# Kernel optimization log

Hardware: AMD Instinct MI355X
Metric: run time of the kernel (lower is better)

Reference implementation:

```python
import jax, jax.numpy as jnp
import numpy as np

NUM_ANCHORS = 3
NUM_CLASSES = 3
NUM_BB_ATTR = 9  # x, y, z, h, w, l, im, re, conf
EXP_CLAMP = 1000.0

_ANCHORS = np.array([[11.4, 8.6, 38.7, 0.0, 1.0],
                     [25.4, 11.2, 52.0, 0.0, 1.0],
                     [41.9, 16.2, 75.2, 0.0, 1.0]], dtype=np.float32)


def setup_inputs() -> dict:
    key = jax.random.key(0)
    B, G = 32, 152
    C = NUM_ANCHORS * (NUM_BB_ATTR + NUM_CLASSES)  # 36
    x = jax.random.normal(key, (B, C, G, G), dtype=jnp.float32)
    anchors = jnp.asarray(_ANCHORS)
    return {"x": x, "anchors": anchors, "img_size": 608}


def reference(x, anchors, img_size):
    B, _, G, _ = x.shape
    nA, nC, nbb = NUM_ANCHORS, NUM_CLASSES, NUM_BB_ATTR
    stride = jnp.asarray(img_size, x.dtype) / G

    # [B, nA, 9+nC, G, G] -> [B, nA, G, G, 9+nC]
    pred = x.reshape(B, nA, nbb + nC, G, G).transpose(0, 1, 3, 4, 2)

    pred_x = jax.nn.sigmoid(pred[..., 0])
    pred_y = jax.nn.sigmoid(pred[..., 1])
    pred_z = jax.nn.sigmoid(pred[..., 2])
    pred_h = pred[..., 3]
    pred_w = pred[..., 4]
    pred_l = pred[..., 5]
    pred_im = pred[..., 6]
    pred_re = pred[..., 7]
    pred_conf = jax.nn.sigmoid(pred[..., 8])
    pred_cls = jax.nn.sigmoid(pred[..., 9:])

    # grid offsets: grid_x varies along last (x) axis, grid_y along row axis
    g = jnp.arange(G, dtype=x.dtype)
    grid_x = g[None, None, None, :]   # [1,1,1,G] broadcasts over rows
    grid_y = g[None, None, :, None]   # [1,1,G,1] broadcasts over cols

    scaled = jnp.concatenate([anchors[:, :3] / stride, anchors[:, 3:]], axis=1)
    anchor_h = scaled[:, 0].reshape(1, nA, 1, 1)
    anchor_w = scaled[:, 1].reshape(1, nA, 1, 1)
    anchor_l = scaled[:, 2].reshape(1, nA, 1, 1)

    bx = pred_x + grid_x
    by = pred_y + grid_y
    bz = pred_z
    bh = jnp.minimum(jnp.exp(pred_h), EXP_CLAMP) * anchor_h
    bw = jnp.minimum(jnp.exp(pred_w), EXP_CLAMP) * anchor_w
    bl = jnp.minimum(jnp.exp(pred_l), EXP_CLAMP) * anchor_l

    N = nA * G * G
    flat = lambda t: t.reshape(B, N, 1)
    output = jnp.concatenate([
        flat(bx) * stride, flat(by) * stride,   # xy in image units
        flat(bz),
        flat(bh) * stride, flat(bw) * stride, flat(bl) * stride,
        flat(pred_im), flat(pred_re),
        flat(pred_conf),
        pred_cls.reshape(B, N, nC),
    ], axis=-1)  # [B, nA*G*G, 9+nC]
    return output
```

## Files before the change

### kernel.cpp

```cpp
#include <hip/hip_runtime.h>
#include <math.h>

#define GDIM 152
#define NA 3
#define GG (GDIM * GDIM)
#define EXP_CLAMP 1000.0f

__device__ __forceinline__ float sigmoidf(float v) {
    return 1.0f / (1.0f + __expf(-v));
}

__global__ __launch_bounds__(256) void yolo_decode_v4s(
    const float* __restrict__ x,
    const float* __restrict__ anchors,
    const int* __restrict__ img_size_p,
    float* __restrict__ out,
    int total4)
{
    int tid = blockIdx.x * blockDim.x + threadIdx.x;
    if (tid >= total4) return;
    int base = tid * 4;

    float stride = (float)(*img_size_p) / (float)GDIM;
    float inv_s = 1.0f / stride;

    int gx0 = base % GDIM;
    int t1  = base / GDIM;
    int gy  = t1 % GDIM;
    int t2  = t1 / GDIM;
    int a   = t2 % NA;
    float gyf = (float)gy;

    const float4* ip = (const float4*)(x + (size_t)t2 * 12 * GG + (size_t)gy * GDIM + gx0);
    const int PS = GG / 4;

    float4 r0  = ip[0 * PS];
    float4 r1  = ip[1 * PS];
    float4 r2  = ip[2 * PS];
    float4 r3  = ip[3 * PS];
    float4 r4  = ip[4 * PS];
    float4 r5  = ip[5 * PS];
    float4 r6  = ip[6 * PS];
    float4 r7  = ip[7 * PS];
    float4 r8  = ip[8 * PS];
    float4 r9  = ip[9 * PS];
    float4 r10 = ip[10 * PS];
    float4 r11 = ip[11 * PS];

    float ah4 = anchors[a * 5 + 0] * inv_s * stride;
    float aw4 = anchors[a * 5 + 1] * inv_s * stride;
    float al4 = anchors[a * 5 + 2] * inv_s * stride;

    float4* op = (float4*)(out + (size_t)base * 12);

#define PROC(J, C)                                                        \
    do {                                                                  \
        float4 o0, o1, o2;                                                \
        o0.x = (sigmoidf(r0.C) + (float)(gx0 + J)) * stride;              \
        o0.y = (sigmoidf(r1.C) + gyf) * stride;                           \
        o0.z = sigmoidf(r2.C);                                            \
        o0.w = fminf(__expf(r3.C), EXP_CLAMP) * ah4;                      \
        o1.x = fminf(__expf(r4.C), EXP_CLAMP) * aw4;                      \
        o1.y = fminf(__expf(r5.C), EXP_CLAMP) * al4;                      \
        o1.z = r6.C;                                                      \
        o1.w = r7.C;                                                      \
        o2.x = sigmoidf(r8.C);                                            \
        o2.y = sigmoidf(r9.C);                                            \
        o2.z = sigmoidf(r10.C);                                           \
        o2.w = sigmoidf(r11.C);                                           \
        op[(J) * 3 + 0] = o0;                                             \
        op[(J) * 3 + 1] = o1;                                             \
        op[(J) * 3 + 2] = o2;                                             \
    } while (0)

    PROC(0, x);
    PROC(1, y);
    PROC(2, z);
    PROC(3, w);
#undef PROC
}

extern "C" void kernel_launch(void* const* d_in, const int* in_sizes, int n_in,
                              void* d_out, int out_size, void* d_ws, size_t ws_size,
                              hipStream_t stream) {
    const float* x        = (const float*)d_in[0];
    const float* anchors  = (const float*)d_in[1];
    const int*   img_size = (const int*)d_in[2];
    float*       out      = (float*)d_out;

    const int B = 32;
    const int total4 = (B * NA * GG) / 4;
    const int block = 256;
    const int grid = (total4 + block - 1) / block;

    yolo_decode_v4s<<<grid, block, 0, stream>>>(x, anchors, img_size, out, total4);
}
```

Baseline: 225.5 us.

## Stage outputs through swizzled LDS for fully coalesced global stores

Each block now handles a 1024-cell tile. Threads write their computed 12-float records into XOR-swizzled shared memory, then after a barrier the block writes the tile out as contiguous float4 stores. This replaces per-thread strided 192-byte writes with coalesced ones. In exchange it uses 48 KB of LDS per block, which limits occupancy, and adds a barrier plus LDS traffic.

```diff
diff --git a/kernel.cpp b/kernel.cpp
--- a/kernel.cpp
+++ b/kernel.cpp
@@ -5,33 +5,38 @@
 #define NA 3
 #define GG (GDIM * GDIM)
 #define EXP_CLAMP 1000.0f
+#define TILE 1024
+#define NTHREADS 256
 
 __device__ __forceinline__ float sigmoidf(float v) {
     return 1.0f / (1.0f + __expf(-v));
 }
 
-__global__ __launch_bounds__(256) void yolo_decode_v4s(
+__device__ __forceinline__ int swz(int e) { return e ^ ((e >> 3) & 7); }
+
+__global__ __launch_bounds__(NTHREADS) void yolo_decode_lds(
     const float* __restrict__ x,
     const float* __restrict__ anchors,
     const int* __restrict__ img_size_p,
-    float* __restrict__ out,
-    int total4)
+    float* __restrict__ out)
 {
-    int tid = blockIdx.x * blockDim.x + threadIdx.x;
-    if (tid >= total4) return;
-    int base = tid * 4;
+    __shared__ float4 sh[3][TILE];
 
-    float stride = (float)(*img_size_p) / (float)GDIM;
-    float inv_s = 1.0f / stride;
+    const int t = threadIdx.x;
+    const int tilebase = blockIdx.x * TILE;
 
-    int gx0 = base % GDIM;
-    int t1  = base / GDIM;
-    int gy  = t1 % GDIM;
-    int t2  = t1 / GDIM;
-    int a   = t2 % NA;
-    float gyf = (float)gy;
+    const float stride = (float)(*img_size_p) / (float)GDIM;
+    const float inv_s = 1.0f / stride;
 
-    const float4* ip = (const float4*)(x + (size_t)t2 * 12 * GG + (size_t)gy * GDIM + gx0);
+    const int cbase = tilebase + 4 * t;
+    const unsigned t2 = (unsigned)cbase / (unsigned)GG;
+    const int pos = cbase - (int)t2 * GG;
+    const int gy  = pos / GDIM;
+    const int gx0 = pos - gy * GDIM;
+    const int a   = (int)(t2 % 3u);
+    const float gyf = (float)gy;
+
+    const float4* ip = (const float4*)x + (size_t)(t2 * 12u) * (GG / 4) + (pos >> 2);
     const int PS = GG / 4;
 
     float4 r0  = ip[0 * PS];
@@ -47,30 +52,29 @@
     float4 r10 = ip[10 * PS];
     float4 r11 = ip[11 * PS];
 
-    float ah4 = anchors[a * 5 + 0] * inv_s * stride;
-    float aw4 = anchors[a * 5 + 1] * inv_s * stride;
-    float al4 = anchors[a * 5 + 2] * inv_s * stride;
+    const float ah = anchors[a * 5 + 0] * inv_s * stride;
+    const float aw = anchors[a * 5 + 1] * inv_s * stride;
+    const float al = anchors[a * 5 + 2] * inv_s * stride;
 
-    float4* op = (float4*)(out + (size_t)base * 12);
-
-#define PROC(J, C)                                                        \
-    do {                                                                  \
-        float4 o0, o1, o2;                                                \
-        o0.x = (sigmoidf(r0.C) + (float)(gx0 + J)) * stride;              \
-        o0.y = (sigmoidf(r1.C) + gyf) * stride;                           \
-        o0.z = sigmoidf(r2.C);                                            \
-        o0.w = fminf(__expf(r3.C), EXP_CLAMP) * ah4;                      \
-        o1.x = fminf(__expf(r4.C), EXP_CLAMP) * aw4;                      \
-        o1.y = fminf(__expf(r5.C), EXP_CLAMP) * al4;                      \
-        o1.z = r6.C;                                                      \
-        o1.w = r7.C;                                                      \
-        o2.x = sigmoidf(r8.C);                                            \
-        o2.y = sigmoidf(r9.C);                                            \
-        o2.z = sigmoidf(r10.C);                                           \
-        o2.w = sigmoidf(r11.C);                                           \
-        op[(J) * 3 + 0] = o0;                                             \
-        op[(J) * 3 + 1] = o1;                                             \
-        op[(J) * 3 + 2] = o2;                                             \
+#define PROC(J, C)                                                       \
+    do {                                                                 \
+        float4 o0, o1, o2;                                               \
+        o0.x = (sigmoidf(r0.C) + (float)(gx0 + J)) * stride;             \
+        o0.y = (sigmoidf(r1.C) + gyf) * stride;                          \
+        o0.z = sigmoidf(r2.C);                                           \
+        o0.w = fminf(__expf(r3.C), EXP_CLAMP) * ah;                      \
+        o1.x = fminf(__expf(r4.C), EXP_CLAMP) * aw;                      \
+        o1.y = fminf(__expf(r5.C), EXP_CLAMP) * al;                      \
+        o1.z = r6.C;                                                     \
+        o1.w = r7.C;                                                     \
+        o2.x = sigmoidf(r8.C);                                           \
+        o2.y = sigmoidf(r9.C);                                           \
+        o2.z = sigmoidf(r10.C);                                          \
+        o2.w = sigmoidf(r11.C);                                          \
+        int e = swz(4 * t + (J));                                        \
+        sh[0][e] = o0;                                                   \
+        sh[1][e] = o1;                                                   \
+        sh[2][e] = o2;                                                   \
     } while (0)
 
     PROC(0, x);
@@ -78,6 +82,17 @@
     PROC(2, z);
     PROC(3, w);
 #undef PROC
+
+    __syncthreads();
+
+    float4* op = (float4*)out + (size_t)tilebase * 3;
+#pragma unroll
+    for (int k = 0; k < 12; ++k) {
+        int F = t + NTHREADS * k;
+        unsigned cell = (unsigned)F / 3u;
+        int g = F - (int)cell * 3;
+        op[F] = sh[g][swz((int)cell)];
+    }
 }
 
 extern "C" void kernel_launch(void* const* d_in, const int* in_sizes, int n_in,
@@ -89,9 +104,8 @@
     float*       out      = (float*)d_out;
 
     const int B = 32;
-    const int total4 = (B * NA * GG) / 4;
-    const int block = 256;
-    const int grid = (total4 + block - 1) / block;
+    const int total = B * NA * GG;
+    const int grid = total / TILE;
 
-    yolo_decode_v4s<<<grid, block, 0, stream>>>(x, anchors, img_size, out, total4);
+    yolo_decode_lds<<<grid, NTHREADS, 0, stream>>>(x, anchors, img_size, out);
 }
```

Measured after the change: 190.0 us. 1.19x faster.
